# Kernel optimization log

Measured on AMD Instinct MI355X. Metric: run time of the kernel, lower is better.

## Reference

```python
import jax, jax.numpy as jnp
import numpy as np

N, DEG, D_COORD, D_CH, D_HID = 20000, 32, 3, 64, 256
E = N * DEG


def setup_inputs() -> dict:
    key = jax.random.key(0)
    ks = jax.random.split(key, 12)
    y = jax.random.normal(ks[0], (N, D_COORD), dtype=jnp.float32)
    x = jax.random.normal(ks[1], (N, D_COORD), dtype=jnp.float32)
    f_y = jax.random.normal(ks[2], (N, D_CH), dtype=jnp.float32)
    # quadrature weights ~ 1/|A(x)| scale
    weights = jax.random.uniform(ks[3], (N,), dtype=jnp.float32) / DEG
    neighbors_index = jax.random.randint(ks[4], (E,), 0, N, dtype=jnp.int32)
    neighbors_row_splits = (jnp.arange(N + 1, dtype=jnp.int32) * DEG)
    d_in = 2 * D_COORD + D_CH  # 70: concat(y_nbr, x_self, f_nbr) for 'nonlinear'
    W1 = jax.random.normal(ks[5], (d_in, D_HID), dtype=jnp.float32) / np.sqrt(d_in)
    b1 = jnp.zeros((D_HID,), dtype=jnp.float32)
    W2 = jax.random.normal(ks[6], (D_HID, D_HID), dtype=jnp.float32) / np.sqrt(D_HID)
    b2 = jnp.zeros((D_HID,), dtype=jnp.float32)
    W3 = jax.random.normal(ks[7], (D_HID, D_CH), dtype=jnp.float32) / np.sqrt(D_HID)
    b3 = jnp.zeros((D_CH,), dtype=jnp.float32)
    return {"y": y, "x": x, "f_y": f_y, "weights": weights,
            "neighbors_index": neighbors_index,
            "neighbors_row_splits": neighbors_row_splits,
            "W1": W1, "b1": b1, "W2": W2, "b2": b2, "W3": W3, "b3": b3}


def reference(y, x, f_y, weights, neighbors_index, neighbors_row_splits,
              W1, b1, W2, b2, W3, b3):
    n = y.shape[0]
    e = neighbors_index.shape[0]
    # CSR -> per-edge segment id (equivalent to torch repeat_interleave(num_reps))
    seg = jnp.searchsorted(neighbors_row_splits, jnp.arange(e), side='right') - 1
    rep_features = y[neighbors_index]      # [E, d1] gathered neighbor coords
    self_features = x[seg]                 # [E, d2] repeated query coords
    in_features = f_y[neighbors_index]     # [E, d3] gathered function values
    # transform_type == 'nonlinear': kernel sees (x, y, f(y))
    agg = jnp.concatenate([rep_features, self_features, in_features], axis=-1)
    h = jax.nn.gelu(agg @ W1 + b1, approximate=False)
    h = jax.nn.gelu(h @ W2 + b2, approximate=False)
    k = h @ W3 + b3                        # [E, d3]
    # (d): k(x,y,f(y)) * f(y), then weighted segment-CSR sum
    msg = weights[neighbors_index][:, None] * (k * in_features)
    out = jax.ops.segment_sum(msg, seg, num_segments=n)  # [n, d3]
    return out[None]  # [1, n, d3] (batch of 1)
```

## Files before the change

### kernel.cpp

```cpp
#include <hip/hip_runtime.h>
#include <math.h>
#include <stdint.h>

#define NN   20000
#define DEG  32
#define DIN  70
#define KP   96
#define DH   256
#define DC   64
#define NT   512
#define ET   128
#define NPB  4

typedef _Float16 f16;
typedef _Float16 f16x4 __attribute__((ext_vector_type(4)));
typedef _Float16 f16x8 __attribute__((ext_vector_type(8)));
typedef float    f32x4 __attribute__((ext_vector_type(4)));

#define AGG_P 104
#define H_P   264

#define W1T_OFF 0
#define W2T_OFF (256*KP)
#define W3T_OFF (256*KP + 256*DH)
#define WS_F16_TOTAL (256*KP + 256*DH + DC*DH)

__device__ __forceinline__ float gelu_fast(float v) {
    float u  = v * 0.70710678118654752f;
    float a  = fabsf(u);
    float t  = __builtin_amdgcn_rcpf(fmaf(0.3275911f, a, 1.0f));
    float p  = fmaf(1.061405429f, t, -1.453152027f);
    p = fmaf(p, t, 1.421413741f);
    p = fmaf(p, t, -0.284496736f);
    p = fmaf(p, t, 0.254829592f);
    p = p * t;
    float e  = __expf(-u * u);
    float er = fmaf(-p, e, 1.0f);
    er = copysignf(er, u);
    return 0.5f * v * (1.0f + er);
}

__device__ __forceinline__ uint32_t pack2h(float a, float b) {
    f16 lo = (f16)a, hi = (f16)b;
    return (uint32_t)__builtin_bit_cast(uint16_t, lo)
         | ((uint32_t)__builtin_bit_cast(uint16_t, hi) << 16);
}

__global__ void prep_weights(const float* __restrict__ W1,
                             const float* __restrict__ W2,
                             const float* __restrict__ W3,
                             f16* __restrict__ ws)
{
    int t = blockIdx.x * blockDim.x + threadIdx.x;
    if (t < W2T_OFF) {
        int n = t / KP, k = t - n * KP;
        ws[t] = (k < DIN) ? (f16)W1[k * DH + n] : (f16)0.0f;
    } else if (t < W3T_OFF) {
        int u = t - W2T_OFF;
        int n = u >> 8, k = u & 255;
        ws[t] = (f16)W2[k * DH + n];
    } else if (t < WS_F16_TOTAL) {
        int u = t - W3T_OFF;
        int n = u >> 8, k = u & 255;
        ws[t] = (f16)W3[k * DC + n];
    }
}

__global__ __launch_bounds__(NT, 4)
void it_mfma_kernel(const float* __restrict__ y,
                    const float* __restrict__ x,
                    const float* __restrict__ f_y,
                    const float* __restrict__ wq,
                    const int*   __restrict__ nbr,
                    const float* __restrict__ b1,
                    const float* __restrict__ b2,
                    const float* __restrict__ b3,
                    const f16*  __restrict__ ws,
                    float* __restrict__ out)
{
    const int blk  = blockIdx.x;
    const int t    = threadIdx.x;
    const int lane = t & 63;
    const int w    = t >> 6;
    const int l15  = lane & 15;
    const int lk   = lane >> 4;

    const f16* w1t = ws + W1T_OFF;
    const f16* w2t = ws + W2T_OFF;
    const f16* w3t = ws + W3T_OFF;

    __shared__ __align__(16) unsigned char s_u[ET * H_P * 2];
    f16 (*s_agg)[AGG_P] = (f16(*)[AGG_P])s_u;
    f16 (*s_h)[H_P]     = (f16(*)[H_P])s_u;
    __shared__ int   s_nbr[ET];
    __shared__ float s_wq[ET];
    __shared__ float s_red[8][DC];

    if (t < ET) {
        int n = nbr[blk * ET + t];
        s_nbr[t] = n;
        s_wq[t]  = wq[n];
    }
    __syncthreads();

    {
        uint32_t* aggu = (uint32_t*)&s_agg[0][0];
        #pragma unroll
        for (int p = 0; p < 8; ++p) {
            int idx = t + p * NT;
            int e   = idx >> 5;
            int c2  = idx & 31;
            int n   = s_nbr[e];
            float2 fvv = *(const float2*)&f_y[n * DC + 2 * c2];
            aggu[e * 52 + 3 + c2] = pack2h(fvv.x, fvv.y);
        }
        if (t < ET) {
            int e = t;
            int n = s_nbr[e];
            int node = blk * NPB + (e >> 5);
            float y0 = y[n*3], y1 = y[n*3+1], y2 = y[n*3+2];
            float x0 = x[node*3], x1 = x[node*3+1], x2 = x[node*3+2];
            aggu[e*52 + 0] = pack2h(y0, y1);
            aggu[e*52 + 1] = pack2h(y2, x0);
            aggu[e*52 + 2] = pack2h(x1, x2);
            #pragma unroll
            for (int c = 35; c < 48; ++c) aggu[e*52 + c] = 0;
        }
    }
    __syncthreads();

    const int m_base = (w >> 2) * 64;
    const int n_base = (w & 3) * 64;

    f32x4 acc[4][4];

    #pragma unroll
    for (int nj = 0; nj < 4; ++nj) {
        float4 bv = *(const float4*)&b1[n_base + nj*16 + lk*4];
        #pragma unroll
        for (int mi = 0; mi < 4; ++mi) acc[mi][nj] = (f32x4){bv.x, bv.y, bv.z, bv.w};
    }
    #pragma unroll
    for (int ks = 0; ks < KP/32; ++ks) {
        const int k0 = ks*32 + lk*8;
        f16x8 a[4], b[4];
        #pragma unroll
        for (int mi = 0; mi < 4; ++mi)
            a[mi] = *(const f16x8*)&s_agg[m_base + mi*16 + l15][k0];
        #pragma unroll
        for (int nj = 0; nj < 4; ++nj)
            b[nj] = *(const f16x8*)&w1t[(n_base + nj*16 + l15) * KP + k0];
        #pragma unroll
        for (int mi = 0; mi < 4; ++mi)
            #pragma unroll
            for (int nj = 0; nj < 4; ++nj)
                acc[mi][nj] = __builtin_amdgcn_mfma_f32_16x16x32_f16(b[nj], a[mi], acc[mi][nj], 0, 0, 0);
    }
    __syncthreads();
    #pragma unroll
    for (int mi = 0; mi < 4; ++mi)
        #pragma unroll
        for (int nj = 0; nj < 4; ++nj) {
            int e  = m_base + mi*16 + l15;
            int n0 = n_base + nj*16 + lk*4;
            f16x4 hv;
            #pragma unroll
            for (int r = 0; r < 4; ++r) hv[r] = (f16)gelu_fast(acc[mi][nj][r]);
            *(f16x4*)&s_h[e][n0] = hv;
        }
    __syncthreads();

    #pragma unroll
    for (int nj = 0; nj < 4; ++nj) {
        float4 bv = *(const float4*)&b2[n_base + nj*16 + lk*4];
        #pragma unroll
        for (int mi = 0; mi < 4; ++mi) acc[mi][nj] = (f32x4){bv.x, bv.y, bv.z, bv.w};
    }
    #pragma unroll 2
    for (int ks = 0; ks < DH/32; ++ks) {
        const int k0 = ks*32 + lk*8;
        f16x8 a[4], b[4];
        #pragma unroll
        for (int mi = 0; mi < 4; ++mi)
            a[mi] = *(const f16x8*)&s_h[m_base + mi*16 + l15][k0];
        #pragma unroll
        for (int nj = 0; nj < 4; ++nj)
            b[nj] = *(const f16x8*)&w2t[(n_base + nj*16 + l15) * DH + k0];
        #pragma unroll
        for (int mi = 0; mi < 4; ++mi)
            #pragma unroll
            for (int nj = 0; nj < 4; ++nj)
                acc[mi][nj] = __builtin_amdgcn_mfma_f32_16x16x32_f16(b[nj], a[mi], acc[mi][nj], 0, 0, 0);
    }
    __syncthreads();
    #pragma unroll
    for (int mi = 0; mi < 4; ++mi)
        #pragma unroll
        for (int nj = 0; nj < 4; ++nj) {
            int e  = m_base + mi*16 + l15;
            int n0 = n_base + nj*16 + lk*4;
            f16x4 hv;
            #pragma unroll
            for (int r = 0; r < 4; ++r) hv[r] = (f16)gelu_fast(acc[mi][nj][r]);
            *(f16x4*)&s_h[e][n0] = hv;
        }
    __syncthreads();

    {
        float fv[4][4]; float wqe[4];
        #pragma unroll
        for (int r = 0; r < 4; ++r) {
            int e = w*16 + lk*4 + r;
            int n = s_nbr[e];
            wqe[r] = s_wq[e];
            #pragma unroll
            for (int nj = 0; nj < 4; ++nj)
                fv[r][nj] = f_y[n * DC + nj*16 + l15];
        }
        f32x4 acc3[4];
        #pragma unroll
        for (int nj = 0; nj < 4; ++nj) {
            float bv = b3[nj*16 + l15];
            acc3[nj] = (f32x4){bv, bv, bv, bv};
        }
        #pragma unroll 2
        for (int ks = 0; ks < DH/32; ++ks) {
            const int k0 = ks*32 + lk*8;
            f16x8 a = *(const f16x8*)&s_h[w*16 + l15][k0];
            #pragma unroll
            for (int nj = 0; nj < 4; ++nj) {
                f16x8 b = *(const f16x8*)&w3t[(nj*16 + l15) * DH + k0];
                acc3[nj] = __builtin_amdgcn_mfma_f32_16x16x32_f16(a, b, acc3[nj], 0, 0, 0);
            }
        }
        float part[4];
        #pragma unroll
        for (int nj = 0; nj < 4; ++nj) {
            float s = 0.f;
            #pragma unroll
            for (int r = 0; r < 4; ++r)
                s = fmaf(wqe[r] * acc3[nj][r], fv[r][nj], s);
            part[nj] = s;
        }
        #pragma unroll
        for (int nj = 0; nj < 4; ++nj) {
            part[nj] += __shfl_xor(part[nj], 16, 64);
            part[nj] += __shfl_xor(part[nj], 32, 64);
        }
        if (lane < 16) {
            #pragma unroll
            for (int nj = 0; nj < 4; ++nj) s_red[w][nj*16 + l15] = part[nj];
        }
    }
    __syncthreads();

    if (t < NPB * DC) {
        int node = t >> 6, c = t & 63;
        out[(blk * NPB + node) * DC + c] = s_red[2*node][c] + s_red[2*node + 1][c];
    }
}

extern "C" void kernel_launch(void* const* d_in, const int* in_sizes, int n_in,
                              void* d_out, int out_size, void* d_ws, size_t ws_size,
                              hipStream_t stream) {
    const float* y   = (const float*)d_in[0];
    const float* x   = (const float*)d_in[1];
    const float* f_y = (const float*)d_in[2];
    const float* wq  = (const float*)d_in[3];
    const int*   nbr = (const int*)d_in[4];
    const float* W1  = (const float*)d_in[6];
    const float* b1  = (const float*)d_in[7];
    const float* W2  = (const float*)d_in[8];
    const float* b2  = (const float*)d_in[9];
    const float* W3  = (const float*)d_in[10];
    const float* b3  = (const float*)d_in[11];
    float* out = (float*)d_out;
    f16*   ws  = (f16*)d_ws;

    hipLaunchKernelGGL(prep_weights, dim3((WS_F16_TOTAL + 255) / 256), dim3(256), 0, stream,
                       W1, W2, W3, ws);
    hipLaunchKernelGGL(it_mfma_kernel, dim3(NN / NPB), dim3(NT), 0, stream,
                       y, x, f_y, wq, nbr, b1, b2, b3, ws, out);
}
```

Baseline: 381.9 us.

## Precompute per-node first-layer projection and replace GELU with shared-memory LUT

Result: slower. 440.4 us (+15.3%).

```diff
diff --git a/kernel.cpp b/kernel.cpp
--- a/kernel.cpp
+++ b/kernel.cpp
@@ -17,13 +17,13 @@
 typedef _Float16 f16x8 __attribute__((ext_vector_type(8)));
 typedef float    f32x4 __attribute__((ext_vector_type(4)));
 
-#define AGG_P 104
-#define H_P   264
-
 #define W1T_OFF 0
 #define W2T_OFF (256*KP)
 #define W3T_OFF (256*KP + 256*DH)
 #define WS_F16_TOTAL (256*KP + 256*DH + DC*DH)
+#define P_OFF   WS_F16_TOTAL
+
+#define LUTE 2049
 
 __device__ __forceinline__ float gelu_fast(float v) {
     float u  = v * 0.70710678118654752f;
@@ -40,10 +40,28 @@
     return 0.5f * v * (1.0f + er);
 }
 
+__device__ __forceinline__ float gelu_lut(const float* __restrict__ lut, float v) {
+    float s  = fmaf(v, 128.0f, 1024.0f);
+    s = fminf(fmaxf(s, 0.0f), 2047.999f);
+    float jf = floorf(s);
+    float fr = s - jf;
+    int j = (int)jf;
+    float a = lut[j], b = lut[j + 1];
+    float g = fmaf(fr, b - a, a);
+    g = (v >  8.0f) ? v    : g;
+    g = (v < -8.0f) ? 0.0f : g;
+    return g;
+}
+
 __device__ __forceinline__ uint32_t pack2h(float a, float b) {
     f16 lo = (f16)a, hi = (f16)b;
     return (uint32_t)__builtin_bit_cast(uint16_t, lo)
          | ((uint32_t)__builtin_bit_cast(uint16_t, hi) << 16);
+}
+
+__device__ __forceinline__ f16* h_at(f16* base, int row, int col) {
+    uint32_t off = (uint32_t)(row << 9) + ((uint32_t)(col << 1) ^ (uint32_t)((row & 7) << 4));
+    return (f16*)((char*)base + off);
 }
 
 __global__ void prep_weights(const float* __restrict__ W1,
@@ -66,17 +84,46 @@
     }
 }
 
+__global__ void prep_P(const float* __restrict__ y,
+                       const float* __restrict__ f_y,
+                       const float* __restrict__ W1,
+                       f16* __restrict__ P)
+{
+    int node = blockIdx.x * 4 + (threadIdx.x >> 6);
+    int lane = threadIdx.x & 63;
+    if (node >= NN) return;
+    int c0 = lane * 4;
+    float4 acc = {0.f, 0.f, 0.f, 0.f};
+    #pragma unroll
+    for (int k = 0; k < 3; ++k) {
+        float yv = y[node * 3 + k];
+        float4 wv = *(const float4*)&W1[k * DH + c0];
+        acc.x = fmaf(yv, wv.x, acc.x); acc.y = fmaf(yv, wv.y, acc.y);
+        acc.z = fmaf(yv, wv.z, acc.z); acc.w = fmaf(yv, wv.w, acc.w);
+    }
+    float fv = f_y[node * DC + lane];
+    #pragma unroll 8
+    for (int j = 0; j < DC; ++j) {
+        float fj = __shfl(fv, j, 64);
+        float4 wv = *(const float4*)&W1[(6 + j) * DH + c0];
+        acc.x = fmaf(fj, wv.x, acc.x); acc.y = fmaf(fj, wv.y, acc.y);
+        acc.z = fmaf(fj, wv.z, acc.z); acc.w = fmaf(fj, wv.w, acc.w);
+    }
+    f16x4 pv; pv[0] = (f16)acc.x; pv[1] = (f16)acc.y; pv[2] = (f16)acc.z; pv[3] = (f16)acc.w;
+    *(f16x4*)&P[(size_t)node * DH + c0] = pv;
+}
+
 __global__ __launch_bounds__(NT, 4)
-void it_mfma_kernel(const float* __restrict__ y,
-                    const float* __restrict__ x,
-                    const float* __restrict__ f_y,
-                    const float* __restrict__ wq,
-                    const int*   __restrict__ nbr,
-                    const float* __restrict__ b1,
-                    const float* __restrict__ b2,
-                    const float* __restrict__ b3,
-                    const f16*  __restrict__ ws,
-                    float* __restrict__ out)
+void it_mfma2_kernel(const float* __restrict__ x,
+                     const float* __restrict__ f_y,
+                     const float* __restrict__ wq,
+                     const int*   __restrict__ nbr,
+                     const float* __restrict__ W1,
+                     const float* __restrict__ b1,
+                     const float* __restrict__ b2,
+                     const float* __restrict__ b3,
+                     const f16*  __restrict__ ws,
+                     float* __restrict__ out)
 {
     const int blk  = blockIdx.x;
     const int t    = threadIdx.x;
@@ -85,55 +132,209 @@
     const int l15  = lane & 15;
     const int lk   = lane >> 4;
 
+    const f16* w2t = ws + W2T_OFF;
+    const f16* w3t = ws + W3T_OFF;
+    const f16* P   = ws + P_OFF;
+
+    __shared__ __align__(16) f16 s_h[ET][DH];
+    __shared__ float s_lut[2052];
+    __shared__ float s_q[NPB][DH];
+    __shared__ int   s_nbr[ET];
+    __shared__ float s_wq[ET];
+    __shared__ float s_red[8][DC];
+    f16* s_h0 = &s_h[0][0];
+
+    if (t < ET) {
+        int n = nbr[blk * ET + t];
+        s_nbr[t] = n;
+        s_wq[t]  = wq[n];
+    }
+    for (int i = t; i < LUTE; i += NT)
+        s_lut[i] = gelu_fast((float)i * 0.0078125f - 8.0f);
+    for (int idx = t; idx < NPB * DH; idx += NT) {
+        int node = idx >> 8, c = idx & 255;
+        int g = blk * NPB + node;
+        float q = b1[c];
+        q = fmaf(x[g * 3 + 0], W1[3 * DH + c], q);
+        q = fmaf(x[g * 3 + 1], W1[4 * DH + c], q);
+        q = fmaf(x[g * 3 + 2], W1[5 * DH + c], q);
+        s_q[node][c] = q;
+    }
+    __syncthreads();
+
+    {
+        const int e    = t >> 2;
+        const int part = t & 3;
+        const int node = e >> 5;
+        const f16* Prow = P + (size_t)s_nbr[e] * DH;
+        #pragma unroll
+        for (int p = 0; p < 8; ++p) {
+            int c = part * 64 + p * 8;
+            f16x8 pv = *(const f16x8*)&Prow[c];
+            f32x4 q0 = *(const f32x4*)&s_q[node][c];
+            f32x4 q1 = *(const f32x4*)&s_q[node][c + 4];
+            f16x8 hv;
+            #pragma unroll
+            for (int j = 0; j < 4; ++j)
+                hv[j] = (f16)gelu_lut(s_lut, (float)pv[j] + q0[j]);
+            #pragma unroll
+            for (int j = 0; j < 4; ++j)
+                hv[4 + j] = (f16)gelu_lut(s_lut, (float)pv[4 + j] + q1[j]);
+            *(f16x8*)h_at(s_h0, e, c) = hv;
+        }
+    }
+    __syncthreads();
+
+    const int m_base = (w >> 2) * 64;
+    const int n_base = (w & 3) * 64;
+
+    f32x4 acc[4][4];
+
+    #pragma unroll
+    for (int nj = 0; nj < 4; ++nj) {
+        float4 bv = *(const float4*)&b2[n_base + nj*16 + lk*4];
+        #pragma unroll
+        for (int mi = 0; mi < 4; ++mi) acc[mi][nj] = (f32x4){bv.x, bv.y, bv.z, bv.w};
+    }
+    #pragma unroll 2
+    for (int ks = 0; ks < DH/32; ++ks) {
+        const int k0 = ks*32 + lk*8;
+        f16x8 a[4], b[4];
+        #pragma unroll
+        for (int mi = 0; mi < 4; ++mi)
+            a[mi] = *(const f16x8*)h_at(s_h0, m_base + mi*16 + l15, k0);
+        #pragma unroll
+        for (int nj = 0; nj < 4; ++nj)
+            b[nj] = *(const f16x8*)&w2t[(n_base + nj*16 + l15) * DH + k0];
+        #pragma unroll
+        for (int mi = 0; mi < 4; ++mi)
+            #pragma unroll
+            for (int nj = 0; nj < 4; ++nj)
+                acc[mi][nj] = __builtin_amdgcn_mfma_f32_16x16x32_f16(b[nj], a[mi], acc[mi][nj], 0, 0, 0);
+    }
+    __syncthreads();
+    #pragma unroll
+    for (int mi = 0; mi < 4; ++mi)
+        #pragma unroll
+        for (int nj = 0; nj < 4; ++nj) {
+            int e  = m_base + mi*16 + l15;
+            int n0 = n_base + nj*16 + lk*4;
+            f16x4 hv;
+            #pragma unroll
+            for (int r = 0; r < 4; ++r) hv[r] = (f16)gelu_lut(s_lut, acc[mi][nj][r]);
+            *(f16x4*)h_at(s_h0, e, n0) = hv;
+        }
+    __syncthreads();
+
+    {
+        float fv[4][4]; float wqe[4];
+        #pragma unroll
+        for (int r = 0; r < 4; ++r) {
+            int e = w*16 + lk*4 + r;
+            int n = s_nbr[e];
+            wqe[r] = s_wq[e];
+            #pragma unroll
+            for (int nj = 0; nj < 4; ++nj)
+                fv[r][nj] = f_y[n * DC + nj*16 + l15];
+        }
+        f32x4 acc3[4];
+        #pragma unroll
+        for (int nj = 0; nj < 4; ++nj) {
+            float bv = b3[nj*16 + l15];
+            acc3[nj] = (f32x4){bv, bv, bv, bv};
+        }
+        #pragma unroll 2
+        for (int ks = 0; ks < DH/32; ++ks) {
+            const int k0 = ks*32 + lk*8;
+            f16x8 a = *(const f16x8*)h_at(s_h0, w*16 + l15, k0);
+            #pragma unroll
+            for (int nj = 0; nj < 4; ++nj) {
+                f16x8 b = *(const f16x8*)&w3t[(nj*16 + l15) * DH + k0];
+                acc3[nj] = __builtin_amdgcn_mfma_f32_16x16x32_f16(a, b, acc3[nj], 0, 0, 0);
+            }
+        }
+        float part[4];
+        #pragma unroll
+        for (int nj = 0; nj < 4; ++nj) {
+            float s = 0.f;
+            #pragma unroll
+            for (int r = 0; r < 4; ++r)
+                s = fmaf(wqe[r] * acc3[nj][r], fv[r][nj], s);
+            part[nj] = s;
+        }
+        #pragma unroll
+        for (int nj = 0; nj < 4; ++nj) {
+            part[nj] += __shfl_xor(part[nj], 16, 64);
+            part[nj] += __shfl_xor(part[nj], 32, 64);
+        }
+        if (lane < 16) {
+            #pragma unroll
+            for (int nj = 0; nj < 4; ++nj) s_red[w][nj*16 + l15] = part[nj];
+        }
+    }
+    __syncthreads();
+
+    if (t < NPB * DC) {
+        int node = t >> 6, c = t & 63;
+        out[(blk * NPB + node) * DC + c] = s_red[2*node][c] + s_red[2*node + 1][c];
+    }
+}
+
+__global__ __launch_bounds__(NT, 4)
+void it_mfma_fallback(const float* __restrict__ y,
+                      const float* __restrict__ x,
+                      const float* __restrict__ f_y,
+                      const float* __restrict__ wq,
+                      const int*   __restrict__ nbr,
+                      const float* __restrict__ b1,
+                      const float* __restrict__ b2,
+                      const float* __restrict__ b3,
+                      const f16*  __restrict__ ws,
+                      float* __restrict__ out)
+{
+    const int blk  = blockIdx.x;
+    const int t    = threadIdx.x;
+    const int lane = t & 63;
+    const int w    = t >> 6;
+    const int l15  = lane & 15;
+    const int lk   = lane >> 4;
     const f16* w1t = ws + W1T_OFF;
     const f16* w2t = ws + W2T_OFF;
     const f16* w3t = ws + W3T_OFF;
-
+    #define AGG_P 104
+    #define H_P   264
     __shared__ __align__(16) unsigned char s_u[ET * H_P * 2];
     f16 (*s_agg)[AGG_P] = (f16(*)[AGG_P])s_u;
     f16 (*s_h)[H_P]     = (f16(*)[H_P])s_u;
     __shared__ int   s_nbr[ET];
     __shared__ float s_wq[ET];
     __shared__ float s_red[8][DC];
-
-    if (t < ET) {
-        int n = nbr[blk * ET + t];
-        s_nbr[t] = n;
-        s_wq[t]  = wq[n];
-    }
-    __syncthreads();
-
+    if (t < ET) { int n = nbr[blk * ET + t]; s_nbr[t] = n; s_wq[t] = wq[n]; }
+    __syncthreads();
     {
         uint32_t* aggu = (uint32_t*)&s_agg[0][0];
         #pragma unroll
         for (int p = 0; p < 8; ++p) {
             int idx = t + p * NT;
-            int e   = idx >> 5;
-            int c2  = idx & 31;
-            int n   = s_nbr[e];
+            int e = idx >> 5, c2 = idx & 31;
+            int n = s_nbr[e];
             float2 fvv = *(const float2*)&f_y[n * DC + 2 * c2];
             aggu[e * 52 + 3 + c2] = pack2h(fvv.x, fvv.y);
         }
         if (t < ET) {
-            int e = t;
-            int n = s_nbr[e];
+            int e = t, n = s_nbr[e];
             int node = blk * NPB + (e >> 5);
-            float y0 = y[n*3], y1 = y[n*3+1], y2 = y[n*3+2];
-            float x0 = x[node*3], x1 = x[node*3+1], x2 = x[node*3+2];
-            aggu[e*52 + 0] = pack2h(y0, y1);
-            aggu[e*52 + 1] = pack2h(y2, x0);
-            aggu[e*52 + 2] = pack2h(x1, x2);
+            aggu[e*52 + 0] = pack2h(y[n*3], y[n*3+1]);
+            aggu[e*52 + 1] = pack2h(y[n*3+2], x[node*3]);
+            aggu[e*52 + 2] = pack2h(x[node*3+1], x[node*3+2]);
             #pragma unroll
             for (int c = 35; c < 48; ++c) aggu[e*52 + c] = 0;
         }
     }
     __syncthreads();
-
     const int m_base = (w >> 2) * 64;
     const int n_base = (w & 3) * 64;
-
     f32x4 acc[4][4];
-
     #pragma unroll
     for (int nj = 0; nj < 4; ++nj) {
         float4 bv = *(const float4*)&b1[n_base + nj*16 + lk*4];
@@ -145,11 +346,9 @@
         const int k0 = ks*32 + lk*8;
         f16x8 a[4], b[4];
         #pragma unroll
-        for (int mi = 0; mi < 4; ++mi)
-            a[mi] = *(const f16x8*)&s_agg[m_base + mi*16 + l15][k0];
-        #pragma unroll
-        for (int nj = 0; nj < 4; ++nj)
-            b[nj] = *(const f16x8*)&w1t[(n_base + nj*16 + l15) * KP + k0];
+        for (int mi = 0; mi < 4; ++mi) a[mi] = *(const f16x8*)&s_agg[m_base + mi*16 + l15][k0];
+        #pragma unroll
+        for (int nj = 0; nj < 4; ++nj) b[nj] = *(const f16x8*)&w1t[(n_base + nj*16 + l15) * KP + k0];
         #pragma unroll
         for (int mi = 0; mi < 4; ++mi)
             #pragma unroll
@@ -161,15 +360,13 @@
     for (int mi = 0; mi < 4; ++mi)
         #pragma unroll
         for (int nj = 0; nj < 4; ++nj) {
-            int e  = m_base + mi*16 + l15;
-            int n0 = n_base + nj*16 + lk*4;
+            int e = m_base + mi*16 + l15, n0 = n_base + nj*16 + lk*4;
             f16x4 hv;
             #pragma unroll
             for (int r = 0; r < 4; ++r) hv[r] = (f16)gelu_fast(acc[mi][nj][r]);
             *(f16x4*)&s_h[e][n0] = hv;
         }
     __syncthreads();
-
     #pragma unroll
     for (int nj = 0; nj < 4; ++nj) {
         float4 bv = *(const float4*)&b2[n_base + nj*16 + lk*4];
@@ -181,11 +378,9 @@
         const int k0 = ks*32 + lk*8;
         f16x8 a[4], b[4];
         #pragma unroll
-        for (int mi = 0; mi < 4; ++mi)
-            a[mi] = *(const f16x8*)&s_h[m_base + mi*16 + l15][k0];
-        #pragma unroll
-        for (int nj = 0; nj < 4; ++nj)
-            b[nj] = *(const f16x8*)&w2t[(n_base + nj*16 + l15) * DH + k0];
+        for (int mi = 0; mi < 4; ++mi) a[mi] = *(const f16x8*)&s_h[m_base + mi*16 + l15][k0];
+        #pragma unroll
+        for (int nj = 0; nj < 4; ++nj) b[nj] = *(const f16x8*)&w2t[(n_base + nj*16 + l15) * DH + k0];
         #pragma unroll
         for (int mi = 0; mi < 4; ++mi)
             #pragma unroll
@@ -197,32 +392,25 @@
     for (int mi = 0; mi < 4; ++mi)
         #pragma unroll
         for (int nj = 0; nj < 4; ++nj) {
-            int e  = m_base + mi*16 + l15;
-            int n0 = n_base + nj*16 + lk*4;
+            int e = m_base + mi*16 + l15, n0 = n_base + nj*16 + lk*4;
             f16x4 hv;
             #pragma unroll
             for (int r = 0; r < 4; ++r) hv[r] = (f16)gelu_fast(acc[mi][nj][r]);
             *(f16x4*)&s_h[e][n0] = hv;
         }
     __syncthreads();
-
     {
         float fv[4][4]; float wqe[4];
         #pragma unroll
         for (int r = 0; r < 4; ++r) {
-            int e = w*16 + lk*4 + r;
-            int n = s_nbr[e];
+            int e = w*16 + lk*4 + r, n = s_nbr[e];
             wqe[r] = s_wq[e];
             #pragma unroll
-            for (int nj = 0; nj < 4; ++nj)
-                fv[r][nj] = f_y[n * DC + nj*16 + l15];
+            for (int nj = 0; nj < 4; ++nj) fv[r][nj] = f_y[n * DC + nj*16 + l15];
         }
         f32x4 acc3[4];
         #pragma unroll
-        for (int nj = 0; nj < 4; ++nj) {
-            float bv = b3[nj*16 + l15];
-            acc3[nj] = (f32x4){bv, bv, bv, bv};
-        }
+        for (int nj = 0; nj < 4; ++nj) { float bv = b3[nj*16 + l15]; acc3[nj] = (f32x4){bv, bv, bv, bv}; }
         #pragma unroll 2
         for (int ks = 0; ks < DH/32; ++ks) {
             const int k0 = ks*32 + lk*8;
@@ -238,8 +426,7 @@
         for (int nj = 0; nj < 4; ++nj) {
             float s = 0.f;
             #pragma unroll
-            for (int r = 0; r < 4; ++r)
-                s = fmaf(wqe[r] * acc3[nj][r], fv[r][nj], s);
+            for (int r = 0; r < 4; ++r) s = fmaf(wqe[r] * acc3[nj][r], fv[r][nj], s);
             part[nj] = s;
         }
         #pragma unroll
@@ -253,7 +440,6 @@
         }
     }
     __syncthreads();
-
     if (t < NPB * DC) {
         int node = t >> 6, c = t & 63;
         out[(blk * NPB + node) * DC + c] = s_red[2*node][c] + s_red[2*node + 1][c];
@@ -279,6 +465,15 @@
 
     hipLaunchKernelGGL(prep_weights, dim3((WS_F16_TOTAL + 255) / 256), dim3(256), 0, stream,
                        W1, W2, W3, ws);
-    hipLaunchKernelGGL(it_mfma_kernel, dim3(NN / NPB), dim3(NT), 0, stream,
-                       y, x, f_y, wq, nbr, b1, b2, b3, ws, out);
-}
+
+    size_t need_bytes = ((size_t)WS_F16_TOTAL + (size_t)NN * DH) * sizeof(f16);
+    if (ws_size >= need_bytes) {
+        hipLaunchKernelGGL(prep_P, dim3((NN + 3) / 4), dim3(256), 0, stream,
+                           y, f_y, W1, ws + P_OFF);
+        hipLaunchKernelGGL(it_mfma2_kernel, dim3(NN / NPB), dim3(NT), 0, stream,
+                           x, f_y, wq, nbr, W1, b1, b2, b3, ws, out);
+    } else {
+        hipLaunchKernelGGL(it_mfma_fallback, dim3(NN / NPB), dim3(NT), 0, stream,
+                           y, x, f_y, wq, nbr, b1, b2, b3, ws, out);
+    }
+}
```

## Pre-pack neighbor f_y and y into fp16 rows and swizzle hidden LDS tile

Applied to the files above, without the earlier changes.

After: 396.7 us. 3.9% more time.

```diff
diff --git a/kernel.cpp b/kernel.cpp
--- a/kernel.cpp
+++ b/kernel.cpp
@@ -18,12 +18,12 @@
 typedef float    f32x4 __attribute__((ext_vector_type(4)));
 
 #define AGG_P 104
-#define H_P   264
+#define YF_P  72
 
 #define W1T_OFF 0
 #define W2T_OFF (256*KP)
 #define W3T_OFF (256*KP + 256*DH)
-#define WS_F16_TOTAL (256*KP + 256*DH + DC*DH)
+#define YF_OFF  (256*KP + 256*DH + DC*DH)
 
 __device__ __forceinline__ float gelu_fast(float v) {
     float u  = v * 0.70710678118654752f;
@@ -40,10 +40,9 @@
     return 0.5f * v * (1.0f + er);
 }
 
-__device__ __forceinline__ uint32_t pack2h(float a, float b) {
-    f16 lo = (f16)a, hi = (f16)b;
-    return (uint32_t)__builtin_bit_cast(uint16_t, lo)
-         | ((uint32_t)__builtin_bit_cast(uint16_t, hi) << 16);
+__device__ __forceinline__ f16* h_at(f16* base, int row, int col) {
+    uint32_t off = (uint32_t)(row << 9) + ((uint32_t)(col << 1) ^ (uint32_t)((row & 7) << 4));
+    return (f16*)((char*)base + off);
 }
 
 __global__ void prep_weights(const float* __restrict__ W1,
@@ -54,22 +53,40 @@
     int t = blockIdx.x * blockDim.x + threadIdx.x;
     if (t < W2T_OFF) {
         int n = t / KP, k = t - n * KP;
-        ws[t] = (k < DIN) ? (f16)W1[k * DH + n] : (f16)0.0f;
+        float v;
+        if (k < 3)              v = W1[(3 + k) * DH + n];
+        else if (k < 8)         v = 0.0f;
+        else if (k < 72)        v = W1[(6 + (k - 8)) * DH + n];
+        else if (k < 75)        v = W1[(k - 72) * DH + n];
+        else                    v = 0.0f;
+        ws[t] = (f16)v;
     } else if (t < W3T_OFF) {
         int u = t - W2T_OFF;
         int n = u >> 8, k = u & 255;
         ws[t] = (f16)W2[k * DH + n];
-    } else if (t < WS_F16_TOTAL) {
+    } else if (t < W3T_OFF + DC * DH) {
         int u = t - W3T_OFF;
         int n = u >> 8, k = u & 255;
         ws[t] = (f16)W3[k * DC + n];
     }
 }
 
+__global__ void prep_yf(const float* __restrict__ y,
+                        const float* __restrict__ f_y,
+                        f16* __restrict__ yf)
+{
+    int idx = blockIdx.x * blockDim.x + threadIdx.x;
+    if (idx >= NN * YF_P) return;
+    int n = idx / YF_P, c = idx - n * YF_P;
+    float v;
+    if (c < DC)          v = f_y[n * DC + c];
+    else if (c < DC + 3) v = y[n * 3 + (c - DC)];
+    else                 v = 0.0f;
+    yf[idx] = (f16)v;
+}
+
 __global__ __launch_bounds__(NT, 4)
-void it_mfma_kernel(const float* __restrict__ y,
-                    const float* __restrict__ x,
-                    const float* __restrict__ f_y,
+void it_mfma_kernel(const float* __restrict__ x,
                     const float* __restrict__ wq,
                     const int*   __restrict__ nbr,
                     const float* __restrict__ b1,
@@ -88,10 +105,11 @@
     const f16* w1t = ws + W1T_OFF;
     const f16* w2t = ws + W2T_OFF;
     const f16* w3t = ws + W3T_OFF;
-
-    __shared__ __align__(16) unsigned char s_u[ET * H_P * 2];
+    const f16* yf  = ws + YF_OFF;
+
+    __shared__ __align__(16) unsigned char s_u[ET * DH * 2];
     f16 (*s_agg)[AGG_P] = (f16(*)[AGG_P])s_u;
-    f16 (*s_h)[H_P]     = (f16(*)[H_P])s_u;
+    f16* s_h0 = (f16*)s_u;
     __shared__ int   s_nbr[ET];
     __shared__ float s_wq[ET];
     __shared__ float s_red[8][DC];
@@ -104,27 +122,25 @@
     __syncthreads();
 
     {
-        uint32_t* aggu = (uint32_t*)&s_agg[0][0];
-        #pragma unroll
-        for (int p = 0; p < 8; ++p) {
-            int idx = t + p * NT;
-            int e   = idx >> 5;
-            int c2  = idx & 31;
-            int n   = s_nbr[e];
-            float2 fvv = *(const float2*)&f_y[n * DC + 2 * c2];
-            aggu[e * 52 + 3 + c2] = pack2h(fvv.x, fvv.y);
-        }
-        if (t < ET) {
-            int e = t;
-            int n = s_nbr[e];
-            int node = blk * NPB + (e >> 5);
-            float y0 = y[n*3], y1 = y[n*3+1], y2 = y[n*3+2];
-            float x0 = x[node*3], x1 = x[node*3+1], x2 = x[node*3+2];
-            aggu[e*52 + 0] = pack2h(y0, y1);
-            aggu[e*52 + 1] = pack2h(y2, x0);
-            aggu[e*52 + 2] = pack2h(x1, x2);
-            #pragma unroll
-            for (int c = 35; c < 48; ++c) aggu[e*52 + c] = 0;
+        const int e    = t >> 2;
+        const int part = t & 3;
+        const f16* yfr = yf + (size_t)s_nbr[e] * YF_P;
+        f16* aggr = &s_agg[e][0];
+        #pragma unroll
+        for (int j = 0; j < 3; ++j) {
+            int ch = part * 3 + j;
+            if (ch == 0) {
+                int node = blk * NPB + (e >> 5);
+                f16x8 v = {};
+                v[0] = (f16)x[node*3 + 0];
+                v[1] = (f16)x[node*3 + 1];
+                v[2] = (f16)x[node*3 + 2];
+                *(f16x8*)&aggr[0] = v;
+            } else if (ch <= 9) {
+                *(f16x8*)&aggr[8*ch] = *(const f16x8*)&yfr[8*(ch-1)];
+            } else {
+                *(f16x8*)&aggr[8*ch] = (f16x8){};
+            }
         }
     }
     __syncthreads();
@@ -166,7 +182,7 @@
             f16x4 hv;
             #pragma unroll
             for (int r = 0; r < 4; ++r) hv[r] = (f16)gelu_fast(acc[mi][nj][r]);
-            *(f16x4*)&s_h[e][n0] = hv;
+            *(f16x4*)h_at(s_h0, e, n0) = hv;
         }
     __syncthreads();
 
@@ -182,7 +198,7 @@
         f16x8 a[4], b[4];
         #pragma unroll
         for (int mi = 0; mi < 4; ++mi)
-            a[mi] = *(const f16x8*)&s_h[m_base + mi*16 + l15][k0];
+            a[mi] = *(const f16x8*)h_at(s_h0, m_base + mi*16 + l15, k0);
         #pragma unroll
         for (int nj = 0; nj < 4; ++nj)
             b[nj] = *(const f16x8*)&w2t[(n_base + nj*16 + l15) * DH + k0];
@@ -202,7 +218,7 @@
             f16x4 hv;
             #pragma unroll
             for (int r = 0; r < 4; ++r) hv[r] = (f16)gelu_fast(acc[mi][nj][r]);
-            *(f16x4*)&s_h[e][n0] = hv;
+            *(f16x4*)h_at(s_h0, e, n0) = hv;
         }
     __syncthreads();
 
@@ -211,11 +227,11 @@
         #pragma unroll
         for (int r = 0; r < 4; ++r) {
             int e = w*16 + lk*4 + r;
-            int n = s_nbr[e];
+            const f16* yfr = yf + (size_t)s_nbr[e] * YF_P;
             wqe[r] = s_wq[e];
             #pragma unroll
             for (int nj = 0; nj < 4; ++nj)
-                fv[r][nj] = f_y[n * DC + nj*16 + l15];
+                fv[r][nj] = (float)yfr[nj*16 + l15];
         }
         f32x4 acc3[4];
         #pragma unroll
@@ -226,7 +242,7 @@
         #pragma unroll 2
         for (int ks = 0; ks < DH/32; ++ks) {
             const int k0 = ks*32 + lk*8;
-            f16x8 a = *(const f16x8*)&s_h[w*16 + l15][k0];
+            f16x8 a = *(const f16x8*)h_at(s_h0, w*16 + l15, k0);
             #pragma unroll
             for (int nj = 0; nj < 4; ++nj) {
                 f16x8 b = *(const f16x8*)&w3t[(nj*16 + l15) * DH + k0];
@@ -277,8 +293,10 @@
     float* out = (float*)d_out;
     f16*   ws  = (f16*)d_ws;
 
-    hipLaunchKernelGGL(prep_weights, dim3((WS_F16_TOTAL + 255) / 256), dim3(256), 0, stream,
+    hipLaunchKernelGGL(prep_weights, dim3((W3T_OFF + DC*DH + 255) / 256), dim3(256), 0, stream,
                        W1, W2, W3, ws);
+    hipLaunchKernelGGL(prep_yf, dim3((NN * YF_P + 255) / 256), dim3(256), 0, stream,
+                       y, f_y, ws + YF_OFF);
     hipLaunchKernelGGL(it_mfma_kernel, dim3(NN / NPB), dim3(NT), 0, stream,
-                       y, x, f_y, wq, nbr, b1, b2, b3, ws, out);
-}
+                       x, wq, nbr, b1, b2, b3, ws, out);
+}
```
